# Kernel tuning notes

Hardware: AMD Instinct MI355X
Metric: run time of the kernel (lower is better)

Reference implementation:

```python
import jax, jax.numpy as jnp
import numpy as np

_SAMPLING_EPS = 1e-5


def setup_inputs() -> dict:
    key = jax.random.key(0)
    ks = jax.random.split(key, 7)
    N, V, H = 256, 128000, 200  # num_seqs, vocab_size, output-history length
    logits = jax.random.normal(ks[0], (N, V), dtype=jnp.float32)
    output_tokens = jax.random.randint(ks[1], (N, H), 0, V, dtype=jnp.int32)
    presence_penalties = jax.random.uniform(ks[2], (N,), jnp.float32, 0.0, 2.0)
    frequency_penalties = jax.random.uniform(ks[3], (N,), jnp.float32, 0.0, 2.0)
    temperatures = jax.random.uniform(ks[4], (N,), jnp.float32, 0.5, 1.5)
    top_ps = jax.random.uniform(ks[5], (N,), jnp.float32, 0.5, 1.0)
    top_ks = jax.random.randint(ks[6], (N,), 1, 1000, dtype=jnp.int32)
    return {
        "logits": logits,
        "presence_penalties": presence_penalties,
        "frequency_penalties": frequency_penalties,
        "temperatures": temperatures,
        "top_ps": top_ps,
        "output_tokens": output_tokens,
        "top_ks": top_ks,
    }


def reference(logits, presence_penalties, frequency_penalties, temperatures,
              top_ps, output_tokens, top_ks):
    N, V = logits.shape

    # ---- _apply_penalties: bincount of previously generated tokens per row ----
    rows = jnp.arange(N)[:, None]  # [N,1] broadcast against [N,H] token ids
    bin_counts = jnp.zeros((N, V), logits.dtype).at[rows, output_tokens].add(1.0)
    # rows are skipped when both penalties are < eps (original builds an index list)
    active = ((presence_penalties >= _SAMPLING_EPS) |
              (frequency_penalties >= _SAMPLING_EPS))[:, None]
    presence_mask = (bin_counts > 0.0).astype(logits.dtype)
    penalty = (frequency_penalties[:, None] * bin_counts
               + presence_penalties[:, None] * presence_mask)
    logits = logits - jnp.where(active, penalty, jnp.zeros((), logits.dtype))

    # ---- temperature scaling + softmax ----
    logits = logits / temperatures[:, None]
    probs = jax.nn.softmax(logits, axis=-1)

    # ---- _apply_top_p_top_k: sort desc, cumsum, mask, unsort ----
    probs_idx = jnp.argsort(-probs, axis=-1)                    # descending order
    probs_sort = jnp.take_along_axis(probs, probs_idx, axis=-1)
    probs_sum = jnp.cumsum(probs_sort, axis=-1)
    top_p_mask = (probs_sum - probs_sort) > top_ps[:, None]     # exclusive cumsum > p
    probs_sort = jnp.where(top_p_mask, 0.0, probs_sort)
    top_k_mask = jnp.arange(V, dtype=top_ks.dtype)[None, :] >= top_ks[:, None]
    probs_sort = jnp.where(top_k_mask, 0.0, probs_sort)
    inv_idx = jnp.argsort(probs_idx, axis=-1)                   # unsort permutation
    filtered_probs = jnp.take_along_axis(probs_sort, inv_idx, axis=-1)
    return filtered_probs
```

## Files before the change

kernel.cpp:

```cpp
#include <hip/hip_runtime.h>
#include <stdint.h>

#define BSHIFT 19
#define NBR 1024
#define BASEB 0x1700
#define HS 512
#define HM 511
#define CAP 4096
#define CAPW 6144
#define NT 1024
#define NT1 256
#define CH 8
#define LCAP 1536
#define CAPTHR 1.75f

typedef unsigned long long ull;

__device__ __forceinline__ void bar_lds() {
    asm volatile("s_waitcnt lgkmcnt(0)" ::: "memory");
    __builtin_amdgcn_s_barrier();
    __builtin_amdgcn_sched_barrier(0);
}
__device__ __forceinline__ void bar_full() {
    asm volatile("s_waitcnt vmcnt(0) lgkmcnt(0)" ::: "memory");
    __builtin_amdgcn_s_barrier();
    __builtin_amdgcn_sched_barrier(0);
}

__device__ __forceinline__ unsigned mono_u32(float x) {
    unsigned b = __float_as_uint(x);
    return (b & 0x80000000u) ? ~b : (b | 0x80000000u);
}
__device__ __forceinline__ float inv_mono(unsigned u) {
    unsigned b = (u & 0x80000000u) ? (u & 0x7fffffffu) : ~u;
    return __uint_as_float(b);
}
__device__ __forceinline__ int relb(unsigned m) {
    int rel = (int)(m >> BSHIFT) - BASEB;
    return rel < 0 ? 0 : (rel > NBR - 1 ? NBR - 1 : rel);
}

__device__ __forceinline__ float compute_x(float l, int cnt,
                                           float pres, float freq, float t) {
    float pen = __fadd_rn(__fmul_rn(freq, (float)cnt), (cnt > 0) ? pres : 0.0f);
    return __fdiv_rn(__fsub_rn(l, pen), t);
}

__device__ __forceinline__ int hash_cnt(unsigned idx, const int* hkey,
                                        const int* hval) {
    unsigned h = (idx * 2654435761u) >> 23;
    while (true) {
        int kk = hkey[h];
        if (kk == (int)idx) return hval[h];
        if (kk == -1) return 0;
        h = (h + 1) & HM;
    }
}

#define SHFL_STAGE(kk, jj) do {                                              \
    int _s = (jj) >> 1;                                                      \
    ull _pA = __shfl_xor(A, _s), _pB = __shfl_xor(B, _s);                    \
    bool _keepmn = (((e0 & (jj)) == 0) == ((e0 & (kk)) != 0));               \
    ull _mnA = (A < _pA) ? A : _pA, _mxA = (A < _pA) ? _pA : A;              \
    ull _mnB = (B < _pB) ? B : _pB, _mxB = (B < _pB) ? _pB : B;              \
    A = _keepmn ? _mnA : _mxA;  B = _keepmn ? _mnB : _mxB;                   \
} while (0)
#define PAIR_STAGE(kk) do {                                                  \
    bool _up = ((e0 & (kk)) != 0);                                           \
    ull _mn = (A < B) ? A : B, _mx = (A < B) ? B : A;                        \
    A = _up ? _mn : _mx;  B = _up ? _mx : _mn;                               \
} while (0)
#define ZDRIB(nn) do {                                                       \
    for (int _z = 0; _z < (nn) && zc < ZITER; ++_z) {                        \
        int _p = tid + zc * NT; if (_p < V4) o4p[_p] = z4; ++zc;             \
    }                                                                        \
} while (0)

__global__ void k_init(float* esum, int* cur, int N) {
    for (int i = threadIdx.x; i < N; i += blockDim.x) { esum[i] = 0.f; cur[i] = 0; }
}

__global__ __launch_bounds__(NT1) void k_stream(
    const float* __restrict__ logits, const float* __restrict__ temps,
    float* __restrict__ esum_ws, int* __restrict__ cur_ws,
    ull* __restrict__ pairs, int capw, int V)
{
    __shared__ ull lbuf[LCAP];
    __shared__ int lcnt_s, base_s;
    int row = blockIdx.y, c = blockIdx.x, tid = threadIdx.x;
    if (tid == 0) lcnt_s = 0;
    __syncthreads();

    int V4 = V >> 2;
    int csz = (V4 + CH - 1) / CH;
    int beg = c * csz, end = beg + csz; if (end > V4) end = V4;
    const float* lrow = logits + (size_t)row * V;
    const float4* l4p = (const float4*)lrow;
    ull* prow = pairs + (size_t)row * (size_t)capw;
    float t = temps[row];
    float r = __fdiv_rn(1.0f, t);
    float es = 0.0f;
    int i = beg + tid;
    for (; i + 7 * NT1 < end; i += 8 * NT1) {
        float4 arr[8];
#pragma unroll
        for (int q = 0; q < 8; ++q) arr[q] = l4p[i + q * NT1];
#pragma unroll
        for (int q = 0; q < 8; ++q) {
            int vb = (i + q * NT1) << 2;
#pragma unroll
            for (int j = 0; j < 4; ++j) {
                float l = (&arr[q].x)[j];
                es += __expf(__fmul_rn(l, r));
                if (l >= CAPTHR) {
                    int pos = atomicAdd(&lcnt_s, 1);
                    if (pos < LCAP)
                        lbuf[pos] = ((ull)__float_as_uint(l) << 32) | (unsigned)(vb + j);
                }
            }
        }
    }
    for (; i < end; i += NT1) {
        float4 A4 = l4p[i];
        int vb = i << 2;
#pragma unroll
        for (int j = 0; j < 4; ++j) {
            float l = (&A4.x)[j];
            es += __expf(__fmul_rn(l, r));
            if (l >= CAPTHR) {
                int pos = atomicAdd(&lcnt_s, 1);
                if (pos < LCAP)
                    lbuf[pos] = ((ull)__float_as_uint(l) << 32) | (unsigned)(vb + j);
            }
        }
    }
    if (c == CH - 1) {
        for (int v = (V4 << 2) + tid; v < V; v += NT1) {
            float l = lrow[v];
            es += __expf(__fmul_rn(l, r));
            if (l >= CAPTHR) {
                int pos = atomicAdd(&lcnt_s, 1);
                if (pos < LCAP)
                    lbuf[pos] = ((ull)__float_as_uint(l) << 32) | (unsigned)v;
            }
        }
    }
    for (int off = 32; off; off >>= 1) es += __shfl_down(es, off);
    if ((tid & 63) == 0) atomicAdd(&esum_ws[row], es);
    __syncthreads();

    int lc = lcnt_s;
    int wr = lc > LCAP ? LCAP : lc;
    if (tid == 0) {
        int add = (lc > LCAP) ? (lc + (1 << 20)) : lc;
        base_s = atomicAdd(&cur_ws[row], add);
    }
    __syncthreads();
    int base = base_s;
    for (int j = tid; j < wr; j += NT1) {
        int pos = base + j;
        if (pos < capw) prow[pos] = lbuf[j];
    }
}

__global__ __launch_bounds__(NT) void k_select(
    const float* __restrict__ logits, const int* __restrict__ tokens,
    const float* __restrict__ pres_v, const float* __restrict__ freq_v,
    const float* __restrict__ temps, const float* __restrict__ topp_v,
    const int* __restrict__ topk_v, int V, int H, float* __restrict__ out,
    const float* __restrict__ esum_ws, const int* __restrict__ cur_ws,
    const ull* __restrict__ pairs, int capw)
{
    __shared__ __align__(16) ull sbuf[CAP];
    __shared__ float se[CAP];
    __shared__ unsigned hc[NBR];
    __shared__ int hkey[HS];
    __shared__ int hval[HS];
    __shared__ int wt_i[16];
    __shared__ float wt_f[16];
    __shared__ float corr_s;
    __shared__ int bstar_s, lcnt_s;

    int row = blockIdx.x, tid = threadIdx.x;
    int lane = tid & 63, wid = tid >> 6;
    hc[tid] = 0u;
    if (tid == 0) { corr_s = 0.f; bstar_s = -1; lcnt_s = 0; }
    for (int i = tid; i < HS; i += NT) { hkey[i] = -1; hval[i] = 0; }
    __syncthreads();

    const int* trow = tokens + (size_t)row * H;
    for (int i = tid; i < H; i += NT) {
        int v = trow[i];
        unsigned h = ((unsigned)v * 2654435761u) >> 23;
        while (true) {
            int prev = atomicCAS(&hkey[h], -1, v);
            if (prev == -1 || prev == v) { atomicAdd(&hval[h], 1); break; }
            h = (h + 1) & HM;
        }
    }
    __syncthreads();

    float t = temps[row], topp = topp_v[row];
    float pres = pres_v[row], freq = freq_v[row];
    int k = topk_v[row];
    int active = (pres >= 1e-5f) || (freq >= 1e-5f);
    float r = __fdiv_rn(1.0f, t);
    const float* lrow = logits + (size_t)row * V;
    float4* o4p = (float4*)(out + (size_t)row * V);
    const float4 z4 = make_float4(0.f, 0.f, 0.f, 0.f);
    int V4 = V >> 2;
    int ZITER = (V4 + NT - 1) / NT;
    int zc = 0;
    float esv = esum_ws[row];
    int raw = cur_ws[row];
    int ccount = raw < capw ? raw : capw;
    const ull* prow = pairs + (size_t)row * (size_t)capw;

    ull pr[6];
#pragma unroll
    for (int q = 0; q < 6; ++q) {
        int j2 = tid + q * NT;
        pr[q] = (j2 < ccount) ? prow[j2] : 0xffffffffffffffffull;
    }

    float corr = 0.0f;
    if (active) {
        for (int s = tid; s < HS; s += NT) {
            int v = hkey[s];
            if (v >= 0) {
                int c = hval[s];
                float l = lrow[v];
                corr += __expf(compute_x(l, c, pres, freq, t))
                      - __expf(__fmul_rn(l, r));
            }
        }
    }
    for (int off = 32; off; off >>= 1) corr += __shfl_down(corr, off);
    if ((tid & 63) == 0) atomicAdd(&corr_s, corr);
    __syncthreads();

    ull sk[6]; int rel6[6];
#pragma unroll
    for (int q = 0; q < 6; ++q) {
        if (pr[q] != 0xffffffffffffffffull) {
            unsigned idx = (unsigned)(pr[q] & 0xffffffffull);
            float l = __uint_as_float((unsigned)(pr[q] >> 32));
            int c = active ? hash_cnt(idx, hkey, hval) : 0;
            float xe = (c > 0) ? compute_x(l, c, pres, freq, t) : __fdiv_rn(l, t);
            unsigned ue = mono_u32(xe);
            int rl = relb(ue);
            atomicAdd(&hc[rl], 1u);
            sk[q] = ((ull)ue << 32) | (unsigned)~idx;
            rel6[q] = rl;
        } else { sk[q] = 0ull; rel6[q] = -1; }
    }
    ZDRIB(2); bar_lds();

    int myc = (int)hc[tid];
    int vs = myc;
#pragma unroll
    for (int off = 1; off < 64; off <<= 1) {
        int o = __shfl_down(vs, off);
        if (lane + off < 64) vs += o;
    }
    if (lane == 0) wt_i[wid] = vs;
    ZDRIB(2); bar_lds();
    int tot = 0;
#pragma unroll
    for (int w = 0; w < 16; ++w) tot += wt_i[w];
    int above = vs - myc;
#pragma unroll
    for (int w = 0; w < 16; ++w) if (w > wid) above += wt_i[w];
    int fb = (tot < k) || (raw > capw) || (capw <= 0);
    if (!fb && (myc + above >= k)) atomicMax(&bstar_s, tid);
    ZDRIB(2); bar_lds();
    int bst_rel = bstar_s < 0 ? 0 : bstar_s;
    int lb_rel = relb(mono_u32(__fdiv_rn(CAPTHR, t)));
    bool skip = (!fb) && (lb_rel < bst_rel);
    float Sp = esv + corr_s;
    int count;

    if (skip) {
        int sb[6], svc = 0;
#pragma unroll
        for (int q = 0; q < 6; ++q) { sb[q] = (rel6[q] >= bst_rel) ? 1 : 0; svc += sb[q]; }
        int vp = svc;
#pragma unroll
        for (int off = 1; off < 64; off <<= 1) {
            int o = __shfl_up(vp, off);
            if (lane >= off) vp += o;
        }
        if (lane == 63) wt_i[wid] = vp;
        ZDRIB(2); bar_lds();
        int pre = vp - svc;
#pragma unroll
        for (int w = 0; w < 16; ++w) if (w < wid) pre += wt_i[w];
        int total = 0;
#pragma unroll
        for (int w = 0; w < 16; ++w) total += wt_i[w];
        int pos = pre;
#pragma unroll
        for (int q = 0; q < 6; ++q)
            if (sb[q]) { if (pos < CAP) sbuf[pos] = sk[q]; ++pos; }
        count = total > CAP ? CAP : total;
        ZDRIB(2); bar_lds();
    } else {
        if (tid == 0) bstar_s = -1;
        hc[tid] = 0u;
        bar_lds();
        for (int v = tid; v < V; v += NT) {
            float l = lrow[v];
            int c = active ? hash_cnt((unsigned)v, hkey, hval) : 0;
            float xe = (c > 0) ? compute_x(l, c, pres, freq, t) : __fdiv_rn(l, t);
            atomicAdd(&hc[relb(mono_u32(xe))], 1u);
        }
        bar_lds();
        myc = (int)hc[tid];
        vs = myc;
#pragma unroll
        for (int off = 1; off < 64; off <<= 1) {
            int o = __shfl_down(vs, off);
            if (lane + off < 64) vs += o;
        }
        if (lane == 0) wt_i[wid] = vs;
        bar_lds();
        above = vs - myc;
#pragma unroll
        for (int w = 0; w < 16; ++w) if (w > wid) above += wt_i[w];
        if (myc + above >= k) atomicMax(&bstar_s, tid);
        bar_lds();
        bst_rel = bstar_s < 0 ? 0 : bstar_s;
        for (int v = tid; v < V; v += NT) {
            float l = lrow[v];
            int c = active ? hash_cnt((unsigned)v, hkey, hval) : 0;
            float xe = (c > 0) ? compute_x(l, c, pres, freq, t) : __fdiv_rn(l, t);
            unsigned ue = mono_u32(xe);
            if (relb(ue) >= bst_rel) {
                int pos = atomicAdd(&lcnt_s, 1);
                if (pos < CAP) sbuf[pos] = ((ull)ue << 32) | (unsigned)~(unsigned)v;
            }
        }
        bar_lds();
        count = lcnt_s > CAP ? CAP : lcnt_s;
    }

    if (count <= 2048) {
        const int M = 2048;
        for (int j = count + tid; j < M; j += NT) sbuf[j] = 0ull;
        ZDRIB(2); bar_lds();
        int e0 = (wid << 7) + (lane << 1);
        ull A = sbuf[e0], B = sbuf[e0 + 1];
        ZDRIB(2);
        for (int kk = 2; kk <= 128; kk <<= 1) {
            for (int jj = kk >> 1; jj >= 2; jj >>= 1) SHFL_STAGE(kk, jj);
            PAIR_STAGE(kk);
        }
        for (int kk = 256; kk <= 2048; kk <<= 1) {
            sbuf[e0] = A; sbuf[e0 + 1] = B;
            ZDRIB(2); bar_lds();
            for (int jj = kk >> 1; jj >= 128; jj >>= 1) {
                for (int i2 = tid; i2 < M; i2 += NT) {
                    int ixj = i2 ^ jj;
                    if (ixj > i2) {
                        ull X = sbuf[i2], Y = sbuf[ixj];
                        bool up = ((i2 & kk) != 0);
                        if ((X > Y) == up) { sbuf[i2] = Y; sbuf[ixj] = X; }
                    }
                }
                ZDRIB(2); bar_lds();
            }
            A = sbuf[e0]; B = sbuf[e0 + 1];
            for (int jj = 64; jj >= 2; jj >>= 1) SHFL_STAGE(kk, jj);
            PAIR_STAGE(kk);
        }
        sbuf[e0] = A; sbuf[e0 + 1] = B;
    } else {
        int m = 1; while (m < count) m <<= 1;
        for (int j = count + tid; j < m; j += NT) sbuf[j] = 0ull;
        bar_lds();
        for (int kk = 2; kk <= m; kk <<= 1) {
            for (int jj = kk >> 1; jj > 0; jj >>= 1) {
                for (int i2 = tid; i2 < m; i2 += NT) {
                    int ixj = i2 ^ jj;
                    if (ixj > i2) {
                        ull X = sbuf[i2], Y = sbuf[ixj];
                        bool up = ((i2 & kk) != 0);
                        if ((X > Y) == up) { sbuf[i2] = Y; sbuf[ixj] = X; }
                    }
                }
                bar_lds();
            }
        }
    }

    for (; zc < ZITER; ++zc) {
        int p = tid + zc * NT;
        if (p < V4) o4p[p] = z4;
    }
    for (int v2 = (V4 << 2) + tid; v2 < V; v2 += NT)
        out[(size_t)row * V + v2] = 0.0f;
    bar_lds();

    for (int j = tid; j < CAP; j += NT)
        se[j] = (j < count) ? __expf(inv_mono((unsigned)(sbuf[j] >> 32))) : 0.0f;
    bar_lds();
    int j0 = tid << 2;
    float e0f = se[j0], e1 = se[j0 + 1], e2 = se[j0 + 2], e3 = se[j0 + 3];
    float c0 = e0f, c1 = c0 + e1, c2 = c1 + e2, c3 = c2 + e3;
    float vf = c3;
#pragma unroll
    for (int off = 1; off < 64; off <<= 1) {
        float o = __shfl_up(vf, off);
        if (lane >= off) vf += o;
    }
    if (lane == 63) wt_f[wid] = vf;
    bar_lds();
    float pre = vf - c3;
#pragma unroll
    for (int w = 0; w < 16; ++w) if (w < wid) pre += wt_f[w];

    bar_full();

    float pS = topp * Sp;
    float inc[4] = {pre + c0, pre + c1, pre + c2, pre + c3};
    float ee[4] = {e0f, e1, e2, e3};
#pragma unroll
    for (int q = 0; q < 4; ++q) {
        int j = j0 + q;
        if (j < count) {
            float e = ee[q];
            float excl = __fsub_rn(inc[q], e);
            if ((j < k) && (excl <= pS)) {
                unsigned idx = ~(unsigned)(sbuf[j] & 0xffffffffull);
                out[(size_t)row * V + idx] = __fdiv_rn(e, Sp);
            }
        }
    }
}

extern "C" void kernel_launch(void* const* d_in, const int* in_sizes, int n_in,
                              void* d_out, int out_size, void* d_ws, size_t ws_size,
                              hipStream_t stream) {
    const float* logits = (const float*)d_in[0];
    const float* pres   = (const float*)d_in[1];
    const float* freq   = (const float*)d_in[2];
    const float* temps  = (const float*)d_in[3];
    const float* topps  = (const float*)d_in[4];
    const int*   tokens = (const int*)d_in[5];
    const int*   topks  = (const int*)d_in[6];
    int N = in_sizes[1];
    int V = in_sizes[0] / N;
    int H = in_sizes[5] / N;
    float* out = (float*)d_out;

    size_t A = ((size_t)N * 4 + 255) & ~(size_t)255;
    float* esum_ws = (float*)d_ws;
    int*   cur_ws  = (int*)((char*)d_ws + A);
    ull*   pairs   = (ull*)((char*)d_ws + 2 * A);
    int capw = 0;
    if (ws_size > 2 * A + 8)
        capw = (int)(((ws_size - 2 * A) / 8) / (size_t)N);
    if (capw > CAPW) capw = CAPW;
    if (capw < 0) capw = 0;

    k_init<<<1, 256, 0, stream>>>(esum_ws, cur_ws, N);
    k_stream<<<dim3(CH, N), NT1, 0, stream>>>(logits, temps, esum_ws, cur_ws,
                                              pairs, capw, V);
    k_select<<<N, NT, 0, stream>>>(logits, tokens, pres, freq, temps, topps,
                                   topks, V, H, out, esum_ws, cur_ws, pairs, capw);
}
```

Before: 282.5 us.

## Move output zeroing into stream kernel and use per-chunk candidate segments

The output row zeroing now happens in the streaming kernel, spread across the 8 chunk blocks per row, instead of being interleaved with the select kernel's sort phases. Per-row atomics for the exp-sum and candidate counter are replaced by per-chunk slots, so the init kernel launch goes away. The select kernel gathers candidates through chunk prefix offsets. This spreads the large zero-write traffic over more blocks and removes atomics and a launch, at the cost of a more complex candidate gather and a smaller per-chunk capacity.

```diff
diff --git a/kernel.cpp b/kernel.cpp
--- a/kernel.cpp
+++ b/kernel.cpp
@@ -7,7 +7,7 @@
 #define HS 512
 #define HM 511
 #define CAP 4096
-#define CAPW 6144
+#define CAPT 6144
 #define NT 1024
 #define NT1 256
 #define CH 8
@@ -18,11 +18,6 @@
 
 __device__ __forceinline__ void bar_lds() {
     asm volatile("s_waitcnt lgkmcnt(0)" ::: "memory");
-    __builtin_amdgcn_s_barrier();
-    __builtin_amdgcn_sched_barrier(0);
-}
-__device__ __forceinline__ void bar_full() {
-    asm volatile("s_waitcnt vmcnt(0) lgkmcnt(0)" ::: "memory");
     __builtin_amdgcn_s_barrier();
     __builtin_amdgcn_sched_barrier(0);
 }
@@ -70,23 +65,15 @@
     ull _mn = (A < B) ? A : B, _mx = (A < B) ? B : A;                        \
     A = _up ? _mn : _mx;  B = _up ? _mx : _mn;                               \
 } while (0)
-#define ZDRIB(nn) do {                                                       \
-    for (int _z = 0; _z < (nn) && zc < ZITER; ++_z) {                        \
-        int _p = tid + zc * NT; if (_p < V4) o4p[_p] = z4; ++zc;             \
-    }                                                                        \
-} while (0)
-
-__global__ void k_init(float* esum, int* cur, int N) {
-    for (int i = threadIdx.x; i < N; i += blockDim.x) { esum[i] = 0.f; cur[i] = 0; }
-}
 
 __global__ __launch_bounds__(NT1) void k_stream(
     const float* __restrict__ logits, const float* __restrict__ temps,
-    float* __restrict__ esum_ws, int* __restrict__ cur_ws,
-    ull* __restrict__ pairs, int capw, int V)
+    float* __restrict__ esum_c, int* __restrict__ cnt_c,
+    ull* __restrict__ pairs, int capw, int V, float* __restrict__ out)
 {
     __shared__ ull lbuf[LCAP];
-    __shared__ int lcnt_s, base_s;
+    __shared__ float wsum[NT1 / 64];
+    __shared__ int lcnt_s;
     int row = blockIdx.y, c = blockIdx.x, tid = threadIdx.x;
     if (tid == 0) lcnt_s = 0;
     __syncthreads();
@@ -96,7 +83,6 @@
     int beg = c * csz, end = beg + csz; if (end > V4) end = V4;
     const float* lrow = logits + (size_t)row * V;
     const float4* l4p = (const float4*)lrow;
-    ull* prow = pairs + (size_t)row * (size_t)capw;
     float t = temps[row];
     float r = __fdiv_rn(1.0f, t);
     float es = 0.0f;
@@ -146,21 +132,29 @@
         }
     }
     for (int off = 32; off; off >>= 1) es += __shfl_down(es, off);
-    if ((tid & 63) == 0) atomicAdd(&esum_ws[row], es);
+    if ((tid & 63) == 0) wsum[tid >> 6] = es;
     __syncthreads();
 
+    int slot = row * CH + c;
     int lc = lcnt_s;
+    if (tid == 0) {
+        float e4 = 0.f;
+#pragma unroll
+        for (int w = 0; w < NT1 / 64; ++w) e4 += wsum[w];
+        esum_c[slot] = e4;
+        cnt_c[slot] = lc;
+    }
+    ull* seg = pairs + (size_t)slot * (size_t)capw;
     int wr = lc > LCAP ? LCAP : lc;
-    if (tid == 0) {
-        int add = (lc > LCAP) ? (lc + (1 << 20)) : lc;
-        base_s = atomicAdd(&cur_ws[row], add);
-    }
-    __syncthreads();
-    int base = base_s;
-    for (int j = tid; j < wr; j += NT1) {
-        int pos = base + j;
-        if (pos < capw) prow[pos] = lbuf[j];
-    }
+    for (int j = tid; j < wr; j += NT1)
+        if (j < capw) seg[j] = lbuf[j];
+
+    float4* o4p = (float4*)(out + (size_t)row * V);
+    const float4 z4 = make_float4(0.f, 0.f, 0.f, 0.f);
+    for (int p = beg + tid; p < end; p += NT1) o4p[p] = z4;
+    if (c == CH - 1)
+        for (int v2 = (V4 << 2) + tid; v2 < V; v2 += NT1)
+            out[(size_t)row * V + v2] = 0.0f;
 }
 
 __global__ __launch_bounds__(NT) void k_select(
@@ -168,7 +162,7 @@
     const float* __restrict__ pres_v, const float* __restrict__ freq_v,
     const float* __restrict__ temps, const float* __restrict__ topp_v,
     const int* __restrict__ topk_v, int V, int H, float* __restrict__ out,
-    const float* __restrict__ esum_ws, const int* __restrict__ cur_ws,
+    const float* __restrict__ esum_c, const int* __restrict__ cnt_c,
     const ull* __restrict__ pairs, int capw)
 {
     __shared__ __align__(16) ull sbuf[CAP];
@@ -206,21 +200,31 @@
     int active = (pres >= 1e-5f) || (freq >= 1e-5f);
     float r = __fdiv_rn(1.0f, t);
     const float* lrow = logits + (size_t)row * V;
-    float4* o4p = (float4*)(out + (size_t)row * V);
-    const float4 z4 = make_float4(0.f, 0.f, 0.f, 0.f);
-    int V4 = V >> 2;
-    int ZITER = (V4 + NT - 1) / NT;
-    int zc = 0;
-    float esv = esum_ws[row];
-    int raw = cur_ws[row];
-    int ccount = raw < capw ? raw : capw;
-    const ull* prow = pairs + (size_t)row * (size_t)capw;
+
+    int off8[CH + 1];
+    off8[0] = 0;
+    bool ovf = (capw <= 0);
+    float esv = 0.f;
+#pragma unroll
+    for (int c = 0; c < CH; ++c) {
+        int cc = cnt_c[row * CH + c];
+        esv += esum_c[row * CH + c];
+        if (cc > capw) { ovf = true; cc = capw < 0 ? 0 : capw; }
+        off8[c + 1] = off8[c] + (cc < 0 ? 0 : cc);
+    }
+    int tot = off8[CH];
 
     ull pr[6];
 #pragma unroll
     for (int q = 0; q < 6; ++q) {
         int j2 = tid + q * NT;
-        pr[q] = (j2 < ccount) ? prow[j2] : 0xffffffffffffffffull;
+        pr[q] = 0xffffffffffffffffull;
+        if (!ovf && j2 < tot && tot <= CAPT) {
+            int c = 0;
+#pragma unroll
+            for (int s = 1; s < CH; ++s) if (j2 >= off8[s]) c = s;
+            pr[q] = pairs[((size_t)(row * CH + c)) * (size_t)capw + (j2 - off8[c])];
+        }
     }
 
     float corr = 0.0f;
@@ -254,7 +258,7 @@
             rel6[q] = rl;
         } else { sk[q] = 0ull; rel6[q] = -1; }
     }
-    ZDRIB(2); bar_lds();
+    bar_lds();
 
     int myc = (int)hc[tid];
     int vs = myc;
@@ -264,16 +268,16 @@
         if (lane + off < 64) vs += o;
     }
     if (lane == 0) wt_i[wid] = vs;
-    ZDRIB(2); bar_lds();
-    int tot = 0;
-#pragma unroll
-    for (int w = 0; w < 16; ++w) tot += wt_i[w];
+    bar_lds();
+    int htot = 0;
+#pragma unroll
+    for (int w = 0; w < 16; ++w) htot += wt_i[w];
     int above = vs - myc;
 #pragma unroll
     for (int w = 0; w < 16; ++w) if (w > wid) above += wt_i[w];
-    int fb = (tot < k) || (raw > capw) || (capw <= 0);
+    int fb = ovf || (tot > CAPT) || (htot < k);
     if (!fb && (myc + above >= k)) atomicMax(&bstar_s, tid);
-    ZDRIB(2); bar_lds();
+    bar_lds();
     int bst_rel = bstar_s < 0 ? 0 : bstar_s;
     int lb_rel = relb(mono_u32(__fdiv_rn(CAPTHR, t)));
     bool skip = (!fb) && (lb_rel < bst_rel);
@@ -291,7 +295,7 @@
             if (lane >= off) vp += o;
         }
         if (lane == 63) wt_i[wid] = vp;
-        ZDRIB(2); bar_lds();
+        bar_lds();
         int pre = vp - svc;
 #pragma unroll
         for (int w = 0; w < 16; ++w) if (w < wid) pre += wt_i[w];
@@ -303,7 +307,7 @@
         for (int q = 0; q < 6; ++q)
             if (sb[q]) { if (pos < CAP) sbuf[pos] = sk[q]; ++pos; }
         count = total > CAP ? CAP : total;
-        ZDRIB(2); bar_lds();
+        bar_lds();
     } else {
         if (tid == 0) bstar_s = -1;
         hc[tid] = 0u;
@@ -347,17 +351,16 @@
     if (count <= 2048) {
         const int M = 2048;
         for (int j = count + tid; j < M; j += NT) sbuf[j] = 0ull;
-        ZDRIB(2); bar_lds();
+        bar_lds();
         int e0 = (wid << 7) + (lane << 1);
         ull A = sbuf[e0], B = sbuf[e0 + 1];
-        ZDRIB(2);
         for (int kk = 2; kk <= 128; kk <<= 1) {
             for (int jj = kk >> 1; jj >= 2; jj >>= 1) SHFL_STAGE(kk, jj);
             PAIR_STAGE(kk);
         }
         for (int kk = 256; kk <= 2048; kk <<= 1) {
             sbuf[e0] = A; sbuf[e0 + 1] = B;
-            ZDRIB(2); bar_lds();
+            bar_lds();
             for (int jj = kk >> 1; jj >= 128; jj >>= 1) {
                 for (int i2 = tid; i2 < M; i2 += NT) {
                     int ixj = i2 ^ jj;
@@ -367,13 +370,14 @@
                         if ((X > Y) == up) { sbuf[i2] = Y; sbuf[ixj] = X; }
                     }
                 }
-                ZDRIB(2); bar_lds();
+                bar_lds();
             }
             A = sbuf[e0]; B = sbuf[e0 + 1];
             for (int jj = 64; jj >= 2; jj >>= 1) SHFL_STAGE(kk, jj);
             PAIR_STAGE(kk);
         }
         sbuf[e0] = A; sbuf[e0 + 1] = B;
+        bar_lds();
     } else {
         int m = 1; while (m < count) m <<= 1;
         for (int j = count + tid; j < m; j += NT) sbuf[j] = 0ull;
@@ -393,14 +397,6 @@
         }
     }
 
-    for (; zc < ZITER; ++zc) {
-        int p = tid + zc * NT;
-        if (p < V4) o4p[p] = z4;
-    }
-    for (int v2 = (V4 << 2) + tid; v2 < V; v2 += NT)
-        out[(size_t)row * V + v2] = 0.0f;
-    bar_lds();
-
     for (int j = tid; j < CAP; j += NT)
         se[j] = (j < count) ? __expf(inv_mono((unsigned)(sbuf[j] >> 32))) : 0.0f;
     bar_lds();
@@ -418,8 +414,6 @@
     float pre = vf - c3;
 #pragma unroll
     for (int w = 0; w < 16; ++w) if (w < wid) pre += wt_f[w];
-
-    bar_full();
 
     float pS = topp * Sp;
     float inc[4] = {pre + c0, pre + c1, pre + c2, pre + c3};
@@ -453,19 +447,19 @@
     int H = in_sizes[5] / N;
     float* out = (float*)d_out;
 
-    size_t A = ((size_t)N * 4 + 255) & ~(size_t)255;
-    float* esum_ws = (float*)d_ws;
-    int*   cur_ws  = (int*)((char*)d_ws + A);
-    ull*   pairs   = (ull*)((char*)d_ws + 2 * A);
+    size_t hdrA = (size_t)N * CH * 4;
+    size_t hdr = (2 * hdrA + 255) & ~(size_t)255;
+    float* esum_c = (float*)d_ws;
+    int*   cnt_c  = (int*)((char*)d_ws + hdrA);
+    ull*   pairs  = (ull*)((char*)d_ws + hdr);
     int capw = 0;
-    if (ws_size > 2 * A + 8)
-        capw = (int)(((ws_size - 2 * A) / 8) / (size_t)N);
-    if (capw > CAPW) capw = CAPW;
+    if (ws_size > hdr + 8)
+        capw = (int)(((ws_size - hdr) / 8) / ((size_t)N * CH));
+    if (capw > LCAP) capw = LCAP;
     if (capw < 0) capw = 0;
 
-    k_init<<<1, 256, 0, stream>>>(esum_ws, cur_ws, N);
-    k_stream<<<dim3(CH, N), NT1, 0, stream>>>(logits, temps, esum_ws, cur_ws,
-                                              pairs, capw, V);
+    k_stream<<<dim3(CH, N), NT1, 0, stream>>>(logits, temps, esum_c, cnt_c,
+                                              pairs, capw, V, out);
     k_select<<<N, NT, 0, stream>>>(logits, tokens, pres, freq, temps, topps,
-                                   topks, V, H, out, esum_ws, cur_ws, pairs, capw);
-}
+                                   topks, V, H, out, esum_c, cnt_c, pairs, capw);
+}
```

New measurement: 297.2 us. 5.2% more time.
